# Optimization experiments

Hardware: AMD Instinct MI355X
Metric: run time of the kernel (lower is better)

## Reference

```python
import jax, jax.numpy as jnp
import numpy as np

EPS = 1e-12  # F.normalize eps

def _l2norm(x, axis=-1):
    n = jnp.linalg.norm(x, axis=axis, keepdims=True)
    return x / jnp.maximum(n, EPS)

def setup_inputs() -> dict:
    key = jax.random.key(0)
    k1, k2 = jax.random.split(key)
    Q, D = 512, 1024
    B, L = 64, 1024
    queries = jax.random.normal(k1, (Q, D), dtype=jnp.float32)
    local_tokens = jax.random.normal(k2, (B, L, D), dtype=jnp.float32)
    return {"queries": queries, "local_tokens": local_tokens}

def reference(queries, local_tokens):
    # sim_op == 'dot', repeat == True, need_attn_weights == False
    D = local_tokens.shape[-1]
    denom = jnp.sqrt(jnp.asarray(D, dtype=queries.dtype))
    # scores: [B, Q, L] == bmm(expand(queries), local_tokens^T) / sqrt(D)
    scores = jnp.einsum('qd,bld->bql', queries, local_tokens) / denom
    attn = jax.nn.softmax(scores, axis=-1)
    # aggregated: [B, Q, D]
    agg = jnp.einsum('bql,bld->bqd', attn, local_tokens)
    # post L2-normalize both sides (query normalize is batch-invariant)
    qn = _l2norm(queries)          # [Q, D]
    aggn = _l2norm(agg)            # [B, Q, D]
    # per-(b,q) dot product -> [B, Q], then transpose -> [Q, B]
    logits = jnp.einsum('qd,bqd->bq', qn, aggn).T
    return logits
```

## Files before the change

### kernel.cpp

```cpp
#include <hip/hip_runtime.h>

#define QN 512
#define DN 1024
#define BN 64
#define LN 1024

typedef _Float16 f16x8 __attribute__((ext_vector_type(8)));
typedef _Float16 f16x4 __attribute__((ext_vector_type(4)));
typedef float f32x4 __attribute__((ext_vector_type(4)));

__global__ __launch_bounds__(256) void k_convert(const float* __restrict__ tok,
                                                 _Float16* __restrict__ T,
                                                 _Float16* __restrict__ TT) {
  __shared__ __align__(16) _Float16 tile[64][68];
  const int b = blockIdx.z;
  const int l0 = blockIdx.y * 64, d0 = blockIdx.x * 64;
  const int tid = threadIdx.x;
  const int rr = tid >> 4;
  const int cq = tid & 15;
  const size_t base = (size_t)b * LN * DN;
#pragma unroll
  for (int p = 0; p < 4; ++p) {
    const int l = p * 16 + rr;
    const float4 v = *(const float4*)(tok + base + (size_t)(l0 + l) * DN + d0 + cq * 4);
    f16x4 hv;
    hv[0] = (_Float16)v.x; hv[1] = (_Float16)v.y; hv[2] = (_Float16)v.z; hv[3] = (_Float16)v.w;
    *(f16x4*)(T + base + (size_t)(l0 + l) * DN + d0 + cq * 4) = hv;
    tile[cq * 4 + 0][l] = hv[0];
    tile[cq * 4 + 1][l] = hv[1];
    tile[cq * 4 + 2][l] = hv[2];
    tile[cq * 4 + 3][l] = hv[3];
  }
  __syncthreads();
  const size_t baseT = (size_t)b * DN * LN;
#pragma unroll
  for (int p = 0; p < 4; ++p) {
    const int d = p * 16 + rr;
    const f16x4 hv = *(const f16x4*)(&tile[d][cq * 4]);
    *(f16x4*)(TT + baseT + (size_t)(d0 + d) * LN + l0 + cq * 4) = hv;
  }
}

__global__ __launch_bounds__(256) void k_queries(const float* __restrict__ q,
                                                 _Float16* __restrict__ Qh,
                                                 float* __restrict__ invqn) {
  const int qr = blockIdx.x;
  const int tid = threadIdx.x;
  const float4 v = *(const float4*)(q + (size_t)qr * DN + tid * 4);
  float ss = v.x * v.x + v.y * v.y + v.z * v.z + v.w * v.w;
#pragma unroll
  for (int off = 1; off < 64; off <<= 1) ss += __shfl_xor(ss, off, 64);
  __shared__ float red[4];
  if ((tid & 63) == 0) red[tid >> 6] = ss;
  __syncthreads();
  const float tot = red[0] + red[1] + red[2] + red[3];
  f16x4 hv;
  hv[0] = (_Float16)v.x; hv[1] = (_Float16)v.y; hv[2] = (_Float16)v.z; hv[3] = (_Float16)v.w;
  *(f16x4*)(Qh + (size_t)qr * DN + tid * 4) = hv;
  if (tid == 0) invqn[qr] = 1.0f / fmaxf(sqrtf(tot), 1e-12f);
}

__device__ __forceinline__ void decode_bq(int g, int& b, int& q0) {
  const int xcd = g & 7;
  const int t = g >> 3;
  const int qt8 = t & 7;
  b = ((t >> 3) << 3) | xcd;
  q0 = qt8 * 64;
}

__global__ __launch_bounds__(512, 2) void k_scores(const _Float16* __restrict__ Qh,
                                                   const _Float16* __restrict__ T,
                                                   _Float16* __restrict__ P,
                                                   float* __restrict__ numv) {
  __shared__ float maxbuf[8][64];
  __shared__ float sumbuf[8][64];
  __shared__ float numbuf[8][64];
  __shared__ float Mbuf[64];
  __shared__ float Rbuf[64];
  int b, q0;
  decode_bq(blockIdx.x, b, q0);
  const int tid = threadIdx.x;
  const int w = tid >> 6, lane = tid & 63, c = lane & 15, quad = lane >> 4;

  f32x4 acc[4][8];
#pragma unroll
  for (int i = 0; i < 4; ++i)
#pragma unroll
    for (int j = 0; j < 8; ++j) acc[i][j] = 0.f;

  const _Float16* __restrict__ Tb = T + (size_t)b * LN * DN;
  const _Float16* __restrict__ Ab = Qh + (size_t)q0 * DN;

  for (int ks2 = 0; ks2 < 16; ++ks2) {
    const int k0 = ks2 * 64 + quad * 8;
    f16x8 bfr[8][2];
#pragma unroll
    for (int lt = 0; lt < 8; ++lt) {
      const _Float16* p = Tb + (size_t)((w * 8 + lt) * 16 + c) * DN + k0;
      bfr[lt][0] = *(const f16x8*)p;
      bfr[lt][1] = *(const f16x8*)(p + 32);
    }
#pragma unroll
    for (int kk = 0; kk < 2; ++kk) {
      f16x8 afr[4];
#pragma unroll
      for (int qt = 0; qt < 4; ++qt)
        afr[qt] = *(const f16x8*)(Ab + (size_t)(qt * 16 + c) * DN + k0 + kk * 32);
#pragma unroll
      for (int qt = 0; qt < 4; ++qt)
#pragma unroll
        for (int lt = 0; lt < 8; ++lt)
          acc[qt][lt] = __builtin_amdgcn_mfma_f32_16x16x32_f16(afr[qt], bfr[lt][kk],
                                                               acc[qt][lt], 0, 0, 0);
    }
  }

  float mx[4][4];
#pragma unroll
  for (int qt = 0; qt < 4; ++qt)
#pragma unroll
    for (int r = 0; r < 4; ++r) {
      float m = acc[qt][0][r];
#pragma unroll
      for (int lt = 1; lt < 8; ++lt) m = fmaxf(m, acc[qt][lt][r]);
      mx[qt][r] = m;
    }
#pragma unroll
  for (int off = 1; off < 16; off <<= 1)
#pragma unroll
    for (int qt = 0; qt < 4; ++qt)
#pragma unroll
      for (int r = 0; r < 4; ++r) mx[qt][r] = fmaxf(mx[qt][r], __shfl_xor(mx[qt][r], off, 64));
  if (c == 0)
#pragma unroll
    for (int qt = 0; qt < 4; ++qt)
#pragma unroll
      for (int r = 0; r < 4; ++r) maxbuf[w][qt * 16 + quad * 4 + r] = mx[qt][r];
  __syncthreads();
  if (tid < 64) {
    float m = maxbuf[0][tid];
#pragma unroll
    for (int ww = 1; ww < 8; ++ww) m = fmaxf(m, maxbuf[ww][tid]);
    Mbuf[tid] = m;
  }
  __syncthreads();

  const float KE = 0.045084220027780106f;
  float Mr[4][4], sl[4][4], nl[4][4];
#pragma unroll
  for (int qt = 0; qt < 4; ++qt)
#pragma unroll
    for (int r = 0; r < 4; ++r) {
      Mr[qt][r] = Mbuf[qt * 16 + quad * 4 + r];
      sl[qt][r] = 0.f;
      nl[qt][r] = 0.f;
    }
#pragma unroll
  for (int qt = 0; qt < 4; ++qt)
#pragma unroll
    for (int lt = 0; lt < 8; ++lt)
#pragma unroll
      for (int r = 0; r < 4; ++r) {
        const float u = acc[qt][lt][r];
        const float p = exp2f((u - Mr[qt][r]) * KE);
        acc[qt][lt][r] = p;
        sl[qt][r] += p;
        nl[qt][r] += p * u;
      }
#pragma unroll
  for (int off = 1; off < 16; off <<= 1)
#pragma unroll
    for (int qt = 0; qt < 4; ++qt)
#pragma unroll
      for (int r = 0; r < 4; ++r) {
        sl[qt][r] += __shfl_xor(sl[qt][r], off, 64);
        nl[qt][r] += __shfl_xor(nl[qt][r], off, 64);
      }
  if (c == 0)
#pragma unroll
    for (int qt = 0; qt < 4; ++qt)
#pragma unroll
      for (int r = 0; r < 4; ++r) {
        sumbuf[w][qt * 16 + quad * 4 + r] = sl[qt][r];
        numbuf[w][qt * 16 + quad * 4 + r] = nl[qt][r];
      }
  __syncthreads();
  if (tid < 64) {
    float S = 0.f, N = 0.f;
#pragma unroll
    for (int ww = 0; ww < 8; ++ww) {
      S += sumbuf[ww][tid];
      N += numbuf[ww][tid];
    }
    Rbuf[tid] = 1.0f / S;
    numv[(size_t)b * QN + q0 + tid] = N / S;
  }
  __syncthreads();

  _Float16* Pb = P + ((size_t)b * QN + q0) * LN;
#pragma unroll
  for (int qt = 0; qt < 4; ++qt)
#pragma unroll
    for (int r = 0; r < 4; ++r) {
      const int row = qt * 16 + quad * 4 + r;
      const float rS = Rbuf[row];
      _Float16* prow = Pb + (size_t)row * LN + c;
#pragma unroll
      for (int lt = 0; lt < 8; ++lt) prow[(w * 8 + lt) * 16] = (_Float16)(acc[qt][lt][r] * rS);
    }
}

__global__ __launch_bounds__(512, 2) void k_agg(const _Float16* __restrict__ P,
                                                const _Float16* __restrict__ TT,
                                                float* __restrict__ norm2) {
  __shared__ float redbuf[8][64];
  int b, q0;
  decode_bq(blockIdx.x, b, q0);
  const int tid = threadIdx.x;
  const int w = tid >> 6, lane = tid & 63, c = lane & 15, quad = lane >> 4;

  f32x4 acc[4][8];
#pragma unroll
  for (int i = 0; i < 4; ++i)
#pragma unroll
    for (int j = 0; j < 8; ++j) acc[i][j] = 0.f;

  const _Float16* __restrict__ Tb = TT + (size_t)b * DN * LN;
  const _Float16* __restrict__ Pb = P + ((size_t)b * QN + q0) * LN;

  for (int ks2 = 0; ks2 < 16; ++ks2) {
    const int k0 = ks2 * 64 + quad * 8;
    f16x8 bfr[8][2];
#pragma unroll
    for (int dt = 0; dt < 8; ++dt) {
      const _Float16* p = Tb + (size_t)((w * 8 + dt) * 16 + c) * LN + k0;
      bfr[dt][0] = *(const f16x8*)p;
      bfr[dt][1] = *(const f16x8*)(p + 32);
    }
#pragma unroll
    for (int kk = 0; kk < 2; ++kk) {
      f16x8 afr[4];
#pragma unroll
      for (int qt = 0; qt < 4; ++qt)
        afr[qt] = *(const f16x8*)(Pb + (size_t)(qt * 16 + c) * LN + k0 + kk * 32);
#pragma unroll
      for (int qt = 0; qt < 4; ++qt)
#pragma unroll
        for (int dt = 0; dt < 8; ++dt)
          acc[qt][dt] = __builtin_amdgcn_mfma_f32_16x16x32_f16(afr[qt], bfr[dt][kk],
                                                               acc[qt][dt], 0, 0, 0);
    }
  }

  float ss[4][4];
#pragma unroll
  for (int qt = 0; qt < 4; ++qt)
#pragma unroll
    for (int r = 0; r < 4; ++r) {
      float s = 0.f;
#pragma unroll
      for (int dt = 0; dt < 8; ++dt) {
        const float v = acc[qt][dt][r];
        s += v * v;
      }
      ss[qt][r] = s;
    }
#pragma unroll
  for (int off = 1; off < 16; off <<= 1)
#pragma unroll
    for (int qt = 0; qt < 4; ++qt)
#pragma unroll
      for (int r = 0; r < 4; ++r) ss[qt][r] += __shfl_xor(ss[qt][r], off, 64);
  if (c == 0)
#pragma unroll
    for (int qt = 0; qt < 4; ++qt)
#pragma unroll
      for (int r = 0; r < 4; ++r) redbuf[w][qt * 16 + quad * 4 + r] = ss[qt][r];
  __syncthreads();
  if (tid < 64) {
    float s = 0.f;
#pragma unroll
    for (int ww = 0; ww < 8; ++ww) s += redbuf[ww][tid];
    norm2[(size_t)b * QN + q0 + tid] = s;
  }
}

__global__ __launch_bounds__(256) void k_final(const float* __restrict__ numv,
                                               const float* __restrict__ norm2,
                                               const float* __restrict__ invqn,
                                               float* __restrict__ out) {
  const int idx = blockIdx.x * 256 + threadIdx.x;
  const int q = idx >> 6, b = idx & 63;
  const float n = numv[(size_t)b * QN + q];
  const float d = sqrtf(norm2[(size_t)b * QN + q]);
  out[idx] = n * invqn[q] / fmaxf(d, 1e-12f);
}

extern "C" void kernel_launch(void* const* d_in, const int* in_sizes, int n_in,
                              void* d_out, int out_size, void* d_ws, size_t ws_size,
                              hipStream_t stream) {
  (void)in_sizes; (void)n_in; (void)out_size; (void)ws_size;
  const float* queries = (const float*)d_in[0];
  const float* tok = (const float*)d_in[1];
  float* out = (float*)d_out;
  char* ws = (char*)d_ws;

  _Float16* TT = (_Float16*)(ws + 0);
  _Float16* T = (_Float16*)(ws + 134217728);
  _Float16* P = (_Float16*)(ws + 268435456);
  _Float16* Qh = (_Float16*)(ws + 335544320);
  float* invqn = (float*)(ws + 336592896);
  float* numv = (float*)(ws + 336594944);
  float* norm2 = (float*)(ws + 336726016);

  hipLaunchKernelGGL(k_convert, dim3(16, 16, 64), dim3(256), 0, stream, tok, T, TT);
  hipLaunchKernelGGL(k_queries, dim3(512), dim3(256), 0, stream, queries, Qh, invqn);
  hipLaunchKernelGGL(k_scores, dim3(512), dim3(512), 0, stream, Qh, T, P, numv);
  hipLaunchKernelGGL(k_agg, dim3(512), dim3(512), 0, stream, P, TT, norm2);
  hipLaunchKernelGGL(k_final, dim3(128), dim3(256), 0, stream, numv, norm2, invqn, out);
}
```

Measured before the change: 781.1 us.

## Stage GEMM operands through double-buffered LDS via direct global-to-LDS DMA

```diff
diff --git a/kernel.cpp b/kernel.cpp
--- a/kernel.cpp
+++ b/kernel.cpp
@@ -1,4 +1,5 @@
 #include <hip/hip_runtime.h>
+#include <stdint.h>
 
 #define QN 512
 #define DN 1024
@@ -8,6 +9,13 @@
 typedef _Float16 f16x8 __attribute__((ext_vector_type(8)));
 typedef _Float16 f16x4 __attribute__((ext_vector_type(4)));
 typedef float f32x4 __attribute__((ext_vector_type(4)));
+
+#define DMA16(gp, lp)                                                        \
+  __builtin_amdgcn_global_load_lds(                                          \
+      (const __attribute__((address_space(1))) uint32_t*)(const void*)(gp),  \
+      (__attribute__((address_space(3))) uint32_t*)(void*)(lp), 16, 0, 0)
+
+#define WAITVM0() asm volatile("s_waitcnt vmcnt(0)" ::: "memory")
 
 __global__ __launch_bounds__(256) void k_convert(const float* __restrict__ tok,
                                                  _Float16* __restrict__ T,
@@ -72,6 +80,8 @@
                                                    const _Float16* __restrict__ T,
                                                    _Float16* __restrict__ P,
                                                    float* __restrict__ numv) {
+  __shared__ __align__(16) _Float16 Bb[2][32768];
+  __shared__ __align__(16) _Float16 As[2][2048];
   __shared__ float maxbuf[8][64];
   __shared__ float sumbuf[8][64];
   __shared__ float numbuf[8][64];
@@ -82,37 +92,54 @@
   const int tid = threadIdx.x;
   const int w = tid >> 6, lane = tid & 63, c = lane & 15, quad = lane >> 4;
 
+  const char* __restrict__ gT = (const char*)(T + (size_t)b * LN * DN);
+  const char* __restrict__ gA = (const char*)(Qh + (size_t)q0 * DN);
+
+  const int r4 = lane >> 2;
+  const int qsw = ((lane & 3) - ((lane >> 3) & 3)) & 3;
+  const char* gBbase = gT + (size_t)(w * 128 + r4) * 2048 + qsw * 16;
+  const char* gAbase = gA + (size_t)(w * 16 + r4) * 2048 + qsw * 16;
+
+  const int bswz = ((quad + ((c >> 1) & 3)) & 3) * 8;
+  const int boff = (w * 128 + c) * 32 + bswz;
+  const int aoff = c * 32 + bswz;
+
   f32x4 acc[4][8];
 #pragma unroll
   for (int i = 0; i < 4; ++i)
 #pragma unroll
     for (int j = 0; j < 8; ++j) acc[i][j] = 0.f;
 
-  const _Float16* __restrict__ Tb = T + (size_t)b * LN * DN;
-  const _Float16* __restrict__ Ab = Qh + (size_t)q0 * DN;
-
-  for (int ks2 = 0; ks2 < 16; ++ks2) {
-    const int k0 = ks2 * 64 + quad * 8;
-    f16x8 bfr[8][2];
+#pragma unroll
+  for (int j = 0; j < 8; ++j) DMA16(gBbase + j * 32768, &Bb[0][(w * 8 + j) * 512]);
+  if (w < 4) DMA16(gAbase, &As[0][w * 512]);
+  WAITVM0();
+  __syncthreads();
+
+  for (int s = 0; s < 32; ++s) {
+    const int cur = s & 1;
+    if (s < 31) {
+      const int sn = s + 1;
+#pragma unroll
+      for (int j = 0; j < 8; ++j)
+        DMA16(gBbase + j * 32768 + sn * 64, &Bb[cur ^ 1][(w * 8 + j) * 512]);
+      if (w < 4) DMA16(gAbase + sn * 64, &As[cur ^ 1][w * 512]);
+    }
+
+    const _Float16* __restrict__ Bp = &Bb[cur][0];
+    const _Float16* __restrict__ Ap = &As[cur][0];
+    f16x8 afr[4];
+#pragma unroll
+    for (int qt = 0; qt < 4; ++qt) afr[qt] = *(const f16x8*)(Ap + aoff + qt * 512);
 #pragma unroll
     for (int lt = 0; lt < 8; ++lt) {
-      const _Float16* p = Tb + (size_t)((w * 8 + lt) * 16 + c) * DN + k0;
-      bfr[lt][0] = *(const f16x8*)p;
-      bfr[lt][1] = *(const f16x8*)(p + 32);
-    }
-#pragma unroll
-    for (int kk = 0; kk < 2; ++kk) {
-      f16x8 afr[4];
+      const f16x8 bv = *(const f16x8*)(Bp + boff + lt * 512);
 #pragma unroll
       for (int qt = 0; qt < 4; ++qt)
-        afr[qt] = *(const f16x8*)(Ab + (size_t)(qt * 16 + c) * DN + k0 + kk * 32);
-#pragma unroll
-      for (int qt = 0; qt < 4; ++qt)
-#pragma unroll
-        for (int lt = 0; lt < 8; ++lt)
-          acc[qt][lt] = __builtin_amdgcn_mfma_f32_16x16x32_f16(afr[qt], bfr[lt][kk],
-                                                               acc[qt][lt], 0, 0, 0);
-    }
+        acc[qt][lt] = __builtin_amdgcn_mfma_f32_16x16x32_f16(afr[qt], bv, acc[qt][lt], 0, 0, 0);
+    }
+    WAITVM0();
+    __syncthreads();
   }
 
   float mx[4][4];
@@ -206,50 +233,69 @@
       const float rS = Rbuf[row];
       _Float16* prow = Pb + (size_t)row * LN + c;
 #pragma unroll
-      for (int lt = 0; lt < 8; ++lt) prow[(w * 8 + lt) * 16] = (_Float16)(acc[qt][lt][r] * rS);
+      for (int lt = 0; lt < 8; ++lt) prow[w * 128 + lt * 16] = (_Float16)(acc[qt][lt][r] * rS);
     }
 }
 
 __global__ __launch_bounds__(512, 2) void k_agg(const _Float16* __restrict__ P,
                                                 const _Float16* __restrict__ TT,
                                                 float* __restrict__ norm2) {
+  __shared__ __align__(16) _Float16 Bb[2][32768];
+  __shared__ __align__(16) _Float16 As[2][2048];
   __shared__ float redbuf[8][64];
   int b, q0;
   decode_bq(blockIdx.x, b, q0);
   const int tid = threadIdx.x;
   const int w = tid >> 6, lane = tid & 63, c = lane & 15, quad = lane >> 4;
 
+  const char* __restrict__ gT = (const char*)(TT + (size_t)b * DN * LN);
+  const char* __restrict__ gA = (const char*)(P + ((size_t)b * QN + q0) * LN);
+
+  const int r4 = lane >> 2;
+  const int qsw = ((lane & 3) - ((lane >> 3) & 3)) & 3;
+  const char* gBbase = gT + (size_t)(w * 128 + r4) * 2048 + qsw * 16;
+  const char* gAbase = gA + (size_t)(w * 16 + r4) * 2048 + qsw * 16;
+
+  const int bswz = ((quad + ((c >> 1) & 3)) & 3) * 8;
+  const int boff = (w * 128 + c) * 32 + bswz;
+  const int aoff = c * 32 + bswz;
+
   f32x4 acc[4][8];
 #pragma unroll
   for (int i = 0; i < 4; ++i)
 #pragma unroll
     for (int j = 0; j < 8; ++j) acc[i][j] = 0.f;
 
-  const _Float16* __restrict__ Tb = TT + (size_t)b * DN * LN;
-  const _Float16* __restrict__ Pb = P + ((size_t)b * QN + q0) * LN;
-
-  for (int ks2 = 0; ks2 < 16; ++ks2) {
-    const int k0 = ks2 * 64 + quad * 8;
-    f16x8 bfr[8][2];
+#pragma unroll
+  for (int j = 0; j < 8; ++j) DMA16(gBbase + j * 32768, &Bb[0][(w * 8 + j) * 512]);
+  if (w < 4) DMA16(gAbase, &As[0][w * 512]);
+  WAITVM0();
+  __syncthreads();
+
+  for (int s = 0; s < 32; ++s) {
+    const int cur = s & 1;
+    if (s < 31) {
+      const int sn = s + 1;
+#pragma unroll
+      for (int j = 0; j < 8; ++j)
+        DMA16(gBbase + j * 32768 + sn * 64, &Bb[cur ^ 1][(w * 8 + j) * 512]);
+      if (w < 4) DMA16(gAbase + sn * 64, &As[cur ^ 1][w * 512]);
+    }
+
+    const _Float16* __restrict__ Bp = &Bb[cur][0];
+    const _Float16* __restrict__ Ap = &As[cur][0];
+    f16x8 afr[4];
+#pragma unroll
+    for (int qt = 0; qt < 4; ++qt) afr[qt] = *(const f16x8*)(Ap + aoff + qt * 512);
 #pragma unroll
     for (int dt = 0; dt < 8; ++dt) {
-      const _Float16* p = Tb + (size_t)((w * 8 + dt) * 16 + c) * LN + k0;
-      bfr[dt][0] = *(const f16x8*)p;
-      bfr[dt][1] = *(const f16x8*)(p + 32);
-    }
-#pragma unroll
-    for (int kk = 0; kk < 2; ++kk) {
-      f16x8 afr[4];
+      const f16x8 bv = *(const f16x8*)(Bp + boff + dt * 512);
 #pragma unroll
       for (int qt = 0; qt < 4; ++qt)
-        afr[qt] = *(const f16x8*)(Pb + (size_t)(qt * 16 + c) * LN + k0 + kk * 32);
-#pragma unroll
-      for (int qt = 0; qt < 4; ++qt)
-#pragma unroll
-        for (int dt = 0; dt < 8; ++dt)
-          acc[qt][dt] = __builtin_amdgcn_mfma_f32_16x16x32_f16(afr[qt], bfr[dt][kk],
-                                                               acc[qt][dt], 0, 0, 0);
-    }
+        acc[qt][dt] = __builtin_amdgcn_mfma_f32_16x16x32_f16(afr[qt], bv, acc[qt][dt], 0, 0, 0);
+    }
+    WAITVM0();
+    __syncthreads();
   }
 
   float ss[4][4];
```

After: 702.3 us. -10.1%, faster.
